# Kernel optimization log

Hardware: AMD Instinct MI355X
Metric: run time of the kernel (lower is better)

Reference implementation:

```python
import jax, jax.numpy as jnp
import numpy as np

N = 50000      # nodes
E = 1000000    # directed edges
G = 1000       # graphs (molecules) in the batch
D_NODE = 133
D_EDGE = 147
D_H = 128
D_OUT = 1


def _lrelu(v):
    # torch.nn.functional.leaky_relu default negative_slope = 0.01
    return jnp.where(v >= 0, v, 0.01 * v)


def setup_inputs() -> dict:
    key = jax.random.key(0)
    ks = jax.random.split(key, 10)
    s = 0.05
    return {
        "x": jax.random.normal(ks[0], (N, D_NODE), jnp.float32),
        "concat_feats": jax.random.normal(ks[1], (E, D_EDGE), jnp.float32),
        "srt_concat_batch": jax.random.randint(ks[2], (E,), 0, N),
        "end_concat_batch": jax.random.randint(ks[3], (E,), 0, N),
        "num_concat_feats": E,
        "batch": jnp.sort(jax.random.randint(ks[4], (N,), 0, G)),
        "W_init": s * jax.random.normal(ks[5], (D_H, D_EDGE), jnp.float32),
        "b_init": jnp.zeros((D_H,), jnp.float32),
        "W_h1": s * jax.random.normal(ks[6], (D_H, D_H), jnp.float32),
        "b_h1": jnp.zeros((D_H,), jnp.float32),
        "W_mol": s * jax.random.normal(ks[7], (D_H, D_H), jnp.float32),
        "b_mol": jnp.zeros((D_H,), jnp.float32),
        "W_out": s * jax.random.normal(ks[8], (D_OUT, D_H), jnp.float32),
        "b_out": jnp.zeros((D_OUT,), jnp.float32),
    }


def reference(x, concat_feats, srt_concat_batch, end_concat_batch,
              num_concat_feats, batch,
              W_init, b_init, W_h1, b_h1, W_mol, b_mol, W_out, b_out):
    n = x.shape[0]

    def mp(h):
        # scatter_add over end nodes, gather at srt nodes, subtract reverse contribution
        agg = jax.ops.segment_sum(h, end_concat_batch, num_segments=n)
        return agg[srt_concat_batch] - h[end_concat_batch]

    h0 = _lrelu(concat_feats @ W_init.T + b_init)                 # [E, D_H]
    h1 = _lrelu(h0 + mp(h0) @ W_h1.T + b_h1)
    h2 = _lrelu(h1 + mp(h1) @ W_h1.T + b_h1)
    h3 = _lrelu(h2 + mp(h2) @ W_h1.T + b_h1)

    h_node = jax.ops.segment_sum(h3, srt_concat_batch, num_segments=n)  # [N, D_H]
    atom_embs = _lrelu(h_node @ W_mol.T + b_mol)
    # F.normalize(p=2, dim=1) with eps=1e-12
    norms = jnp.maximum(jnp.linalg.norm(atom_embs, axis=1, keepdims=True), 1e-12)
    hg = jax.ops.segment_sum(atom_embs / norms, batch, num_segments=G)  # [G, D_H]
    out = hg @ W_out.T + b_out                                          # [G, D_OUT]
    return (out, atom_embs)
```

## Files before the change

### kernel.cpp

```cpp
#include <hip/hip_runtime.h>

#define NN 50000
#define NE 1000000
#define NG 1000
#define KE 147
#define DH 128

using u16 = unsigned short;
typedef __attribute__((ext_vector_type(8))) short bf16x8;
typedef __attribute__((ext_vector_type(4))) float f32x4;

__device__ __forceinline__ float lrelu(float v){ return fmaxf(v, 0.01f*v); }
__device__ __forceinline__ float bf2f(u16 u){ unsigned int x = ((unsigned int)u)<<16; float f; __builtin_memcpy(&f,&x,4); return f; }
__device__ __forceinline__ u16 f2bf(float f){ unsigned int x; __builtin_memcpy(&x,&f,4); x += 0x7fffu + ((x>>16)&1u); return (u16)(x>>16); }
__device__ __forceinline__ float bflo(unsigned w){ unsigned x = w<<16; float f; __builtin_memcpy(&f,&x,4); return f; }
__device__ __forceinline__ float bfhi(unsigned w){ unsigned x = w & 0xffff0000u; float f; __builtin_memcpy(&f,&x,4); return f; }
__device__ __forceinline__ unsigned pk2(float lo, float hi){ return ((unsigned)f2bf(hi)<<16) | (unsigned)f2bf(lo); }
__device__ __host__ __forceinline__ int cpi(int p){ return (p & 64) | ((p & 3) << 4) | ((p & 63) >> 2); }

__global__ __launch_bounds__(256) void hist_kernel(const int* __restrict__ endi, const int* __restrict__ srt,
                                                   int* __restrict__ cntE, int* __restrict__ cntS){
  for (int i = blockIdx.x*256 + threadIdx.x; i < NE; i += gridDim.x*256){
    atomicAdd(&cntE[endi[i]], 1);
    atomicAdd(&cntS[srt[i]], 1);
  }
}

__global__ __launch_bounds__(1024) void scan2_kernel(const int* __restrict__ cntE, int* __restrict__ offE,
                                                     const int* __restrict__ cntS, int* __restrict__ offS){
  const int* deg = blockIdx.x ? cntS : cntE;
  int* off = blockIdx.x ? offS : offE;
  __shared__ int wsum[17];
  const int t = threadIdx.x, lane = t & 63, wv = t >> 6;
  int carry = 0;
  for (int base = 0; base < 50176; base += 1024){
    const int i = base + t;
    int v = (i < NN) ? deg[i] : 0;
    int s = v;
    #pragma unroll
    for (int d = 1; d < 64; d <<= 1){
      int x = __shfl_up(s, d);
      if (lane >= d) s += x;
    }
    if (lane == 63) wsum[wv] = s;
    __syncthreads();
    if (t == 0){
      int run = 0;
      #pragma unroll
      for (int k = 0; k < 16; ++k){ int x = wsum[k]; wsum[k] = run; run += x; }
      wsum[16] = run;
    }
    __syncthreads();
    if (i <= NN) off[i] = carry + wsum[wv] + s - v;
    carry += wsum[16];
    __syncthreads();
  }
}

__global__ __launch_bounds__(256) void scatter_kernel(const int* __restrict__ endi, const int* __restrict__ srt,
                                                      int* __restrict__ curE, int* __restrict__ curS,
                                                      int* __restrict__ rankE, int* __restrict__ srtE,
                                                      int* __restrict__ listS2, int* __restrict__ endS){
  for (int i = blockIdx.x*256 + threadIdx.x; i < NE; i += gridDim.x*256){
    const int e = endi[i], s = srt[i];
    int p = atomicAdd(&curE[e], 1);
    rankE[i] = p; srtE[p] = s;
    int q = atomicAdd(&curS[s], 1);
    listS2[q] = p; endS[q] = e;
  }
}

__global__ __launch_bounds__(256) void convertW_kernel(const float* __restrict__ W1, const float* __restrict__ W0,
                                                       const float* __restrict__ b0, const float* __restrict__ b1,
                                                       u16* __restrict__ Wb1, u16* __restrict__ Wb0,
                                                       float* __restrict__ bp0, float* __restrict__ bp1){
  int i = blockIdx.x*256 + threadIdx.x;
  if (i < 128*128){
    int j = i >> 7, k = i & 127;
    Wb1[i] = f2bf(W1[j*DH + cpi(k)]);
  }
  if (i < 128*160){
    int j = i/160, k = i - j*160;
    Wb0[i] = (k < KE) ? f2bf(W0[j*KE + k]) : (u16)0;
  }
  if (i < 128){ bp0[i] = b0[cpi(i)]; bp1[i] = b1[cpi(i)]; }
}

__global__ __launch_bounds__(256) void layer0_mfma(const float* __restrict__ cf, const u16* __restrict__ Wb0,
                                                   const float* __restrict__ bp0, const int* __restrict__ rankE,
                                                   u16* __restrict__ h){
  __shared__ __align__(16) u16 As[64*168];
  const int t = threadIdx.x, lane = t & 63, wv = t >> 6;
  const int wr = wv >> 1, wc = wv & 1;
  const int e0 = blockIdx.x * 64;
  const int q = lane & 15, kg8 = (lane >> 4)*8;

  bf16x8 bfrag[5][4];
  #pragma unroll
  for (int fc = 0; fc < 4; ++fc)
    #pragma unroll
    for (int ks = 0; ks < 5; ++ks)
      bfrag[ks][fc] = *(const bf16x8*)&Wb0[(size_t)(wc*64 + fc*16 + q)*160 + ks*32 + kg8];

  {
    const float4* src = (const float4*)(cf + (size_t)e0*KE);
    #pragma unroll
    for (int k = 0; k < 10; ++k){
      const int i4 = t + k*256;
      if (i4 < 2352){
        float4 v = src[i4];
        const int g = i4*4;
        int r = (unsigned)g / 147u;
        int c = g - r*147;
        u16 w0 = f2bf(v.x), w1 = f2bf(v.y), w2 = f2bf(v.z), w3 = f2bf(v.w);
        As[r*168 + c] = w0; if (++c == 147){ c = 0; ++r; }
        As[r*168 + c] = w1; if (++c == 147){ c = 0; ++r; }
        As[r*168 + c] = w2; if (++c == 147){ c = 0; ++r; }
        As[r*168 + c] = w3;
      }
    }
  }
  for (int idx = t; idx < 64*16; idx += 256){
    const int r = idx >> 4, c = idx & 15;
    if (c < 13) As[r*168 + 147 + c] = 0;
  }
  __syncthreads();

  f32x4 acc[2][4];
  #pragma unroll
  for (int fr = 0; fr < 2; ++fr)
    #pragma unroll
    for (int fc = 0; fc < 4; ++fc){ acc[fr][fc][0]=0.f; acc[fr][fc][1]=0.f; acc[fr][fc][2]=0.f; acc[fr][fc][3]=0.f; }
  #pragma unroll
  for (int ks = 0; ks < 5; ++ks){
    bf16x8 a[2];
    #pragma unroll
    for (int fr = 0; fr < 2; ++fr)
      a[fr] = *(const bf16x8*)&As[(wr*32 + fr*16 + q)*168 + ks*32 + kg8];
    #pragma unroll
    for (int fr = 0; fr < 2; ++fr)
      #pragma unroll
      for (int fc = 0; fc < 4; ++fc)
        acc[fr][fc] = __builtin_amdgcn_mfma_f32_16x16x32_bf16(a[fr], bfrag[ks][fc], acc[fr][fc], 0, 0, 0);
  }

  const float4 bb = *(const float4*)&bp0[wc*64 + q*4];
  #pragma unroll
  for (int fr = 0; fr < 2; ++fr){
    #pragma unroll
    for (int r = 0; r < 4; ++r){
      const int ee = e0 + wr*32 + fr*16 + (lane>>4)*4 + r;
      const int row = rankE[ee];
      ushort4 o;
      o.x = f2bf(lrelu(acc[fr][0][r] + bb.x));
      o.y = f2bf(lrelu(acc[fr][1][r] + bb.y));
      o.z = f2bf(lrelu(acc[fr][2][r] + bb.z));
      o.w = f2bf(lrelu(acc[fr][3][r] + bb.w));
      *(ushort4*)&h[(size_t)row*DH + wc*64 + q*4] = o;
    }
  }
}

__global__ __launch_bounds__(256) void aggE_kernel(const u16* __restrict__ h, const int* __restrict__ off,
                                                   float* __restrict__ agg){
  const int t = threadIdx.x, lane = t & 63, wv = t >> 6;
  const int n = blockIdx.x*2 + (wv >> 1);
  const int half = wv & 1;
  const int lo = off[n], hi = off[n+1];
  const int c8 = half*64 + (lane & 7)*8, sub = lane >> 3;
  float a0=0,a1=0,a2=0,a3=0,a4=0,a5=0,a6=0,a7=0;
  for (int i = lo + sub; i < hi; i += 8){
    uint4 hv = *(const uint4*)&h[(size_t)i*DH + c8];
    a0 += bflo(hv.x); a1 += bfhi(hv.x); a2 += bflo(hv.y); a3 += bfhi(hv.y);
    a4 += bflo(hv.z); a5 += bfhi(hv.z); a6 += bflo(hv.w); a7 += bfhi(hv.w);
  }
  a0 += __shfl_xor(a0,8);  a1 += __shfl_xor(a1,8);  a2 += __shfl_xor(a2,8);  a3 += __shfl_xor(a3,8);
  a4 += __shfl_xor(a4,8);  a5 += __shfl_xor(a5,8);  a6 += __shfl_xor(a6,8);  a7 += __shfl_xor(a7,8);
  a0 += __shfl_xor(a0,16); a1 += __shfl_xor(a1,16); a2 += __shfl_xor(a2,16); a3 += __shfl_xor(a3,16);
  a4 += __shfl_xor(a4,16); a5 += __shfl_xor(a5,16); a6 += __shfl_xor(a6,16); a7 += __shfl_xor(a7,16);
  a0 += __shfl_xor(a0,32); a1 += __shfl_xor(a1,32); a2 += __shfl_xor(a2,32); a3 += __shfl_xor(a3,32);
  a4 += __shfl_xor(a4,32); a5 += __shfl_xor(a5,32); a6 += __shfl_xor(a6,32); a7 += __shfl_xor(a7,32);
  if (sub == 0){
    *(float4*)&agg[(size_t)n*DH + c8]     = make_float4(a0,a1,a2,a3);
    *(float4*)&agg[(size_t)n*DH + c8 + 4] = make_float4(a4,a5,a6,a7);
  }
}

__global__ __launch_bounds__(256) void pq_gemm(const float* __restrict__ agg, const u16* __restrict__ h,
                                               const int* __restrict__ rankE, const u16* __restrict__ Wb1,
                                               const float* __restrict__ bp1, u16* __restrict__ P,
                                               u16* __restrict__ Q){
  __shared__ u16 Alds[128][136];
  const int t = threadIdx.x, lane = t & 63, wv = t >> 6;
  const int wr = wv >> 1, wc = wv & 1;
  const int r0 = blockIdx.x * 128;
  const int q = lane & 15, kg8 = (lane >> 4)*8;

  bf16x8 bfrag[4][4];
  #pragma unroll
  for (int fc = 0; fc < 4; ++fc)
    #pragma unroll
    for (int ks = 0; ks < 4; ++ks)
      bfrag[ks][fc] = *(const bf16x8*)&Wb1[(size_t)(wc*64 + fc*16 + q)*128 + ks*32 + kg8];

  {
    const int rt = t >> 1, half = t & 1;
    const int gr = r0 + rt;
    u16* dst = &Alds[rt][half*64];
    if (gr < NN){
      const float4* src = (const float4*)&agg[(size_t)gr*DH + half*64];
      #pragma unroll
      for (int p = 0; p < 16; ++p){
        float4 x = src[p];
        ushort4 o; o.x=f2bf(x.x); o.y=f2bf(x.y); o.z=f2bf(x.z); o.w=f2bf(x.w);
        *(ushort4*)&dst[p*4] = o;
      }
    } else if (gr < 2*NN){
      const int row = rankE[gr - NN];
      const ushort4* src = (const ushort4*)&h[(size_t)row*DH + half*64];
      #pragma unroll
      for (int p = 0; p < 16; ++p) *(ushort4*)&dst[p*4] = src[p];
    } else {
      ushort4 z; z.x=0; z.y=0; z.z=0; z.w=0;
      #pragma unroll
      for (int p = 0; p < 16; ++p) *(ushort4*)&dst[p*4] = z;
    }
  }
  __syncthreads();

  f32x4 acc[4][4];
  #pragma unroll
  for (int fr = 0; fr < 4; ++fr)
    #pragma unroll
    for (int fc = 0; fc < 4; ++fc){ acc[fr][fc][0]=0.f; acc[fr][fc][1]=0.f; acc[fr][fc][2]=0.f; acc[fr][fc][3]=0.f; }
  #pragma unroll
  for (int ks = 0; ks < 4; ++ks){
    bf16x8 a[4];
    #pragma unroll
    for (int fr = 0; fr < 4; ++fr)
      a[fr] = *(const bf16x8*)&Alds[wr*64 + fr*16 + q][ks*32 + kg8];
    #pragma unroll
    for (int fr = 0; fr < 4; ++fr)
      #pragma unroll
      for (int fc = 0; fc < 4; ++fc)
        acc[fr][fc] = __builtin_amdgcn_mfma_f32_16x16x32_bf16(a[fr], bfrag[ks][fc], acc[fr][fc], 0, 0, 0);
  }

  const float4 bb = *(const float4*)&bp1[wc*64 + q*4];
  #pragma unroll
  for (int fr = 0; fr < 4; ++fr){
    #pragma unroll
    for (int r = 0; r < 4; ++r){
      const int grow = r0 + wr*64 + fr*16 + (lane>>4)*4 + r;
      if (grow < NN){
        ushort4 o;
        o.x = f2bf(acc[fr][0][r] + bb.x);
        o.y = f2bf(acc[fr][1][r] + bb.y);
        o.z = f2bf(acc[fr][2][r] + bb.z);
        o.w = f2bf(acc[fr][3][r] + bb.w);
        *(ushort4*)&P[(size_t)grow*DH + wc*64 + q*4] = o;
      } else if (grow < 2*NN){
        ushort4 o;
        o.x = f2bf(acc[fr][0][r]);
        o.y = f2bf(acc[fr][1][r]);
        o.z = f2bf(acc[fr][2][r]);
        o.w = f2bf(acc[fr][3][r]);
        *(ushort4*)&Q[(size_t)(grow-NN)*DH + wc*64 + q*4] = o;
      }
    }
  }
}

__global__ __launch_bounds__(256) void fused_mid(u16* __restrict__ h, const u16* __restrict__ P,
                                                 const u16* __restrict__ Q, const int* __restrict__ srtE,
                                                 const int* __restrict__ off, float* __restrict__ agg){
  const int t = threadIdx.x, lane = t & 63, wv = t >> 6;
  const int n = blockIdx.x*2 + (wv >> 1);
  const int half = wv & 1;
  const int lo = off[n], hi = off[n+1];
  const int c8 = half*64 + (lane & 7)*8, sub = lane >> 3;
  const uint4 qw = *(const uint4*)&Q[(size_t)n*DH + c8];
  const float q0 = bflo(qw.x), q1 = bfhi(qw.x), q2 = bflo(qw.y), q3 = bfhi(qw.y);
  const float q4 = bflo(qw.z), q5 = bfhi(qw.z), q6 = bflo(qw.w), q7 = bfhi(qw.w);
  float a0=0,a1=0,a2=0,a3=0,a4=0,a5=0,a6=0,a7=0;
  for (int i = lo + sub; i < hi; i += 8){
    const int s = srtE[i];
    uint4 hv = *(const uint4*)&h[(size_t)i*DH + c8];
    uint4 pw = *(const uint4*)&P[(size_t)s*DH + c8];
    float v0 = lrelu(bflo(hv.x) + bflo(pw.x) - q0);
    float v1 = lrelu(bfhi(hv.x) + bfhi(pw.x) - q1);
    float v2 = lrelu(bflo(hv.y) + bflo(pw.y) - q2);
    float v3 = lrelu(bfhi(hv.y) + bfhi(pw.y) - q3);
    float v4 = lrelu(bflo(hv.z) + bflo(pw.z) - q4);
    float v5 = lrelu(bfhi(hv.z) + bfhi(pw.z) - q5);
    float v6 = lrelu(bflo(hv.w) + bflo(pw.w) - q6);
    float v7 = lrelu(bfhi(hv.w) + bfhi(pw.w) - q7);
    uint4 o;
    o.x = pk2(v0, v1); o.y = pk2(v2, v3); o.z = pk2(v4, v5); o.w = pk2(v6, v7);
    *(uint4*)&h[(size_t)i*DH + c8] = o;
    a0+=v0; a1+=v1; a2+=v2; a3+=v3; a4+=v4; a5+=v5; a6+=v6; a7+=v7;
  }
  a0 += __shfl_xor(a0,8);  a1 += __shfl_xor(a1,8);  a2 += __shfl_xor(a2,8);  a3 += __shfl_xor(a3,8);
  a4 += __shfl_xor(a4,8);  a5 += __shfl_xor(a5,8);  a6 += __shfl_xor(a6,8);  a7 += __shfl_xor(a7,8);
  a0 += __shfl_xor(a0,16); a1 += __shfl_xor(a1,16); a2 += __shfl_xor(a2,16); a3 += __shfl_xor(a3,16);
  a4 += __shfl_xor(a4,16); a5 += __shfl_xor(a5,16); a6 += __shfl_xor(a6,16); a7 += __shfl_xor(a7,16);
  a0 += __shfl_xor(a0,32); a1 += __shfl_xor(a1,32); a2 += __shfl_xor(a2,32); a3 += __shfl_xor(a3,32);
  a4 += __shfl_xor(a4,32); a5 += __shfl_xor(a5,32); a6 += __shfl_xor(a6,32); a7 += __shfl_xor(a7,32);
  if (sub == 0){
    *(float4*)&agg[(size_t)n*DH + c8]     = make_float4(a0,a1,a2,a3);
    *(float4*)&agg[(size_t)n*DH + c8 + 4] = make_float4(a4,a5,a6,a7);
  }
}

__global__ __launch_bounds__(256) void fused_last(const u16* __restrict__ h, const u16* __restrict__ P,
                                                  const u16* __restrict__ Q, const int* __restrict__ endS,
                                                  const int* __restrict__ listS2, const int* __restrict__ off,
                                                  float* __restrict__ hnode){
  const int t = threadIdx.x, lane = t & 63, wv = t >> 6;
  const int s = blockIdx.x*2 + (wv >> 1);
  const int half = wv & 1;
  const int lo = off[s], hi = off[s+1];
  const int c8 = half*64 + (lane & 7)*8, sub = lane >> 3;
  const uint4 pw = *(const uint4*)&P[(size_t)s*DH + c8];
  const float p0 = bflo(pw.x), p1 = bfhi(pw.x), p2 = bflo(pw.y), p3 = bfhi(pw.y);
  const float p4 = bflo(pw.z), p5 = bfhi(pw.z), p6 = bflo(pw.w), p7 = bfhi(pw.w);
  float a0=0,a1=0,a2=0,a3=0,a4=0,a5=0,a6=0,a7=0;
  for (int i = lo + sub; i < hi; i += 8){
    const int row = listS2[i];
    const int d = endS[i];
    uint4 hv = *(const uint4*)&h[(size_t)row*DH + c8];
    uint4 qw = *(const uint4*)&Q[(size_t)d*DH + c8];
    a0 += lrelu(bflo(hv.x) + p0 - bflo(qw.x));
    a1 += lrelu(bfhi(hv.x) + p1 - bfhi(qw.x));
    a2 += lrelu(bflo(hv.y) + p2 - bflo(qw.y));
    a3 += lrelu(bfhi(hv.y) + p3 - bfhi(qw.y));
    a4 += lrelu(bflo(hv.z) + p4 - bflo(qw.z));
    a5 += lrelu(bfhi(hv.z) + p5 - bfhi(qw.z));
    a6 += lrelu(bflo(hv.w) + p6 - bflo(qw.w));
    a7 += lrelu(bfhi(hv.w) + p7 - bfhi(qw.w));
  }
  a0 += __shfl_xor(a0,8);  a1 += __shfl_xor(a1,8);  a2 += __shfl_xor(a2,8);  a3 += __shfl_xor(a3,8);
  a4 += __shfl_xor(a4,8);  a5 += __shfl_xor(a5,8);  a6 += __shfl_xor(a6,8);  a7 += __shfl_xor(a7,8);
  a0 += __shfl_xor(a0,16); a1 += __shfl_xor(a1,16); a2 += __shfl_xor(a2,16); a3 += __shfl_xor(a3,16);
  a4 += __shfl_xor(a4,16); a5 += __shfl_xor(a5,16); a6 += __shfl_xor(a6,16); a7 += __shfl_xor(a7,16);
  a0 += __shfl_xor(a0,32); a1 += __shfl_xor(a1,32); a2 += __shfl_xor(a2,32); a3 += __shfl_xor(a3,32);
  a4 += __shfl_xor(a4,32); a5 += __shfl_xor(a5,32); a6 += __shfl_xor(a6,32); a7 += __shfl_xor(a7,32);
  if (sub == 0){
    *(float4*)&hnode[(size_t)s*DH + c8]     = make_float4(a0,a1,a2,a3);
    *(float4*)&hnode[(size_t)s*DH + c8 + 4] = make_float4(a4,a5,a6,a7);
  }
}

__global__ __launch_bounds__(256) void node_kernel(
    const float* __restrict__ hn, const float* __restrict__ W,
    const float* __restrict__ b, float* __restrict__ atom, float* __restrict__ normed)
{
  __shared__ float Wt[64*132];
  __shared__ float ms[32*DH];
  const int t = threadIdx.x;
  const int r0 = blockIdx.x * 32;
  const int jg = t & 31, eg = t >> 5;
  for (int idx = t; idx < 32*DH; idx += 256) {
    const int r = r0 + (idx >> 7);
    ms[idx] = (r < NN) ? hn[(size_t)r*DH + (idx & 127)] : 0.f;
  }
  float acc[4][4] = {};
  for (int c = 0; c < 2; ++c) {
    __syncthreads();
    for (int idx = t; idx < 128*64; idx += 256) {
      const int j = idx >> 6, kl = idx & 63;
      Wt[kl*132 + j] = W[j*DH + c*64 + ((kl&3)*16 + (kl>>2))];
    }
    __syncthreads();
    #pragma unroll 4
    for (int kl = 0; kl < 64; ++kl) {
      const float4 w = *(const float4*)&Wt[kl*132 + jg*4];
      const int kg = c*64 + kl;
      #pragma unroll
      for (int i = 0; i < 4; ++i) {
        const float mv = ms[(eg*4+i)*DH + kg];
        acc[i][0] += mv*w.x; acc[i][1] += mv*w.y; acc[i][2] += mv*w.z; acc[i][3] += mv*w.w;
      }
    }
  }
  float bj[4];
  #pragma unroll
  for (int c2 = 0; c2 < 4; ++c2) bj[c2] = b[jg*4 + c2];
  #pragma unroll
  for (int i = 0; i < 4; ++i) {
    const int r = r0 + eg*4 + i;
    float v[4]; float ss = 0.f;
    #pragma unroll
    for (int c2 = 0; c2 < 4; ++c2) { v[c2] = lrelu(acc[i][c2] + bj[c2]); ss += v[c2]*v[c2]; }
    ss += __shfl_xor(ss, 1); ss += __shfl_xor(ss, 2); ss += __shfl_xor(ss, 4);
    ss += __shfl_xor(ss, 8); ss += __shfl_xor(ss, 16);
    if (r < NN) {
      *(float4*)&atom[(size_t)r*DH + jg*4] = make_float4(v[0],v[1],v[2],v[3]);
      const float inv = 1.f / fmaxf(sqrtf(ss), 1e-12f);
      *(float4*)&normed[(size_t)r*DH + jg*4] = make_float4(v[0]*inv,v[1]*inv,v[2]*inv,v[3]*inv);
    }
  }
}

__global__ __launch_bounds__(128) void graph_out_kernel(const float* __restrict__ normed, const int* __restrict__ batch,
                                                        const float* __restrict__ Wo, const float* __restrict__ bo,
                                                        float* __restrict__ out){
  const int g = blockIdx.x, t = threadIdx.x;
  int lo, hi;
  { int a=0, bb=NN; while(a<bb){ int m=(a+bb)>>1; if (batch[m] < g) a=m+1; else bb=m; } lo=a; }
  { int a=lo, bb=NN; while(a<bb){ int m=(a+bb)>>1; if (batch[m] < g+1) a=m+1; else bb=m; } hi=a; }
  float s = 0.f;
  for (int n = lo; n < hi; ++n) s += normed[(size_t)n*DH + t];
  float v = s * Wo[t];
  #pragma unroll
  for (int d2 = 1; d2 < 64; d2 <<= 1) v += __shfl_xor(v, d2);
  __shared__ float red[2];
  if ((t & 63) == 0) red[t >> 6] = v;
  __syncthreads();
  if (t == 0) out[g] = red[0] + red[1] + bo[0];
}

extern "C" void kernel_launch(void* const* d_in, const int* in_sizes, int n_in,
                              void* d_out, int out_size, void* d_ws, size_t ws_size,
                              hipStream_t stream)
{
  const float* cf     = (const float*)d_in[1];
  const int*   srt    = (const int*)d_in[2];
  const int*   endi   = (const int*)d_in[3];
  const int*   batch  = (const int*)d_in[5];
  const float* W_init = (const float*)d_in[6];
  const float* b_init = (const float*)d_in[7];
  const float* W_h1   = (const float*)d_in[8];
  const float* b_h1   = (const float*)d_in[9];
  const float* W_mol  = (const float*)d_in[10];
  const float* b_mol  = (const float*)d_in[11];
  const float* W_out  = (const float*)d_in[12];
  const float* b_out  = (const float*)d_in[13];

  float* out  = (float*)d_out;
  float* atom = out + NG;

  char* ws = (char*)d_ws;
  u16*   h      = (u16*)(ws);
  float* agg    = (float*)(ws + 256000000);
  u16*   P      = (u16*)(ws + 281600000);
  u16*   Q      = (u16*)(ws + 307200000);
  int*   srtE   = (int*)(ws + 332800000);
  int*   endS   = (int*)(ws + 336800000);
  int*   rankE  = (int*)(ws + 340800000);
  int*   listS2 = (int*)(ws + 344800000);
  int*   offE   = (int*)(ws + 348800000);
  int*   offS   = (int*)(ws + 349000704);
  int*   curE   = (int*)(ws + 349201408);
  int*   curS   = (int*)(ws + 349402112);
  u16*   Wb1    = (u16*)(ws + 349602816);
  u16*   Wb0    = (u16*)(ws + 349635584);
  float* bp0    = (float*)(ws + 349676544);
  float* bp1    = (float*)(ws + 349677056);
  float* hnode  = agg;
  float* normed = (float*)(ws);

  hipMemsetAsync(curE, 0, 200704, stream);
  hipMemsetAsync(curS, 0, 200704, stream);
  hist_kernel<<<1024, 256, 0, stream>>>(endi, srt, curE, curS);
  scan2_kernel<<<2, 1024, 0, stream>>>(curE, offE, curS, offS);
  hipMemcpyAsync(curE, offE, (size_t)NN*4, hipMemcpyDeviceToDevice, stream);
  hipMemcpyAsync(curS, offS, (size_t)NN*4, hipMemcpyDeviceToDevice, stream);
  scatter_kernel<<<1024, 256, 0, stream>>>(endi, srt, curE, curS, rankE, srtE, listS2, endS);
  convertW_kernel<<<80, 256, 0, stream>>>(W_h1, W_init, b_init, b_h1, Wb1, Wb0, bp0, bp1);

  layer0_mfma<<<NE/64, 256, 0, stream>>>(cf, Wb0, bp0, rankE, h);
  aggE_kernel<<<NN/2, 256, 0, stream>>>(h, offE, agg);

  for (int l = 0; l < 2; ++l){
    pq_gemm<<<(2*NN + 127)/128, 256, 0, stream>>>(agg, h, rankE, Wb1, bp1, P, Q);
    fused_mid<<<NN/2, 256, 0, stream>>>(h, P, Q, srtE, offE, agg);
  }
  pq_gemm<<<(2*NN + 127)/128, 256, 0, stream>>>(agg, h, rankE, Wb1, bp1, P, Q);
  fused_last<<<NN/2, 256, 0, stream>>>(h, P, Q, endS, listS2, offS, hnode);

  node_kernel<<<(NN + 31)/32, 256, 0, stream>>>(hnode, W_mol, b_mol, atom, normed);
  graph_out_kernel<<<NG, 128, 0, stream>>>(normed, batch, W_out, b_out, out);
}
```

Baseline: 1.038 ms.

## Skip h2 writeback, recompute it on the fly; MFMA node GEMM with atomic graph pooling

```diff
diff --git a/kernel.cpp b/kernel.cpp
--- a/kernel.cpp
+++ b/kernel.cpp
@@ -71,13 +71,16 @@
 }
 
 __global__ __launch_bounds__(256) void convertW_kernel(const float* __restrict__ W1, const float* __restrict__ W0,
+                                                       const float* __restrict__ Wm,
                                                        const float* __restrict__ b0, const float* __restrict__ b1,
                                                        u16* __restrict__ Wb1, u16* __restrict__ Wb0,
+                                                       u16* __restrict__ Wbm,
                                                        float* __restrict__ bp0, float* __restrict__ bp1){
   int i = blockIdx.x*256 + threadIdx.x;
   if (i < 128*128){
     int j = i >> 7, k = i & 127;
     Wb1[i] = f2bf(W1[j*DH + cpi(k)]);
+    Wbm[i] = f2bf(Wm[j*DH + cpi(k)]);
   }
   if (i < 128*160){
     int j = i/160, k = i - j*160;
@@ -220,6 +223,104 @@
       const ushort4* src = (const ushort4*)&h[(size_t)row*DH + half*64];
       #pragma unroll
       for (int p = 0; p < 16; ++p) *(ushort4*)&dst[p*4] = src[p];
+    } else {
+      ushort4 z; z.x=0; z.y=0; z.z=0; z.w=0;
+      #pragma unroll
+      for (int p = 0; p < 16; ++p) *(ushort4*)&dst[p*4] = z;
+    }
+  }
+  __syncthreads();
+
+  f32x4 acc[4][4];
+  #pragma unroll
+  for (int fr = 0; fr < 4; ++fr)
+    #pragma unroll
+    for (int fc = 0; fc < 4; ++fc){ acc[fr][fc][0]=0.f; acc[fr][fc][1]=0.f; acc[fr][fc][2]=0.f; acc[fr][fc][3]=0.f; }
+  #pragma unroll
+  for (int ks = 0; ks < 4; ++ks){
+    bf16x8 a[4];
+    #pragma unroll
+    for (int fr = 0; fr < 4; ++fr)
+      a[fr] = *(const bf16x8*)&Alds[wr*64 + fr*16 + q][ks*32 + kg8];
+    #pragma unroll
+    for (int fr = 0; fr < 4; ++fr)
+      #pragma unroll
+      for (int fc = 0; fc < 4; ++fc)
+        acc[fr][fc] = __builtin_amdgcn_mfma_f32_16x16x32_bf16(a[fr], bfrag[ks][fc], acc[fr][fc], 0, 0, 0);
+  }
+
+  const float4 bb = *(const float4*)&bp1[wc*64 + q*4];
+  #pragma unroll
+  for (int fr = 0; fr < 4; ++fr){
+    #pragma unroll
+    for (int r = 0; r < 4; ++r){
+      const int grow = r0 + wr*64 + fr*16 + (lane>>4)*4 + r;
+      if (grow < NN){
+        ushort4 o;
+        o.x = f2bf(acc[fr][0][r] + bb.x);
+        o.y = f2bf(acc[fr][1][r] + bb.y);
+        o.z = f2bf(acc[fr][2][r] + bb.z);
+        o.w = f2bf(acc[fr][3][r] + bb.w);
+        *(ushort4*)&P[(size_t)grow*DH + wc*64 + q*4] = o;
+      } else if (grow < 2*NN){
+        ushort4 o;
+        o.x = f2bf(acc[fr][0][r]);
+        o.y = f2bf(acc[fr][1][r]);
+        o.z = f2bf(acc[fr][2][r]);
+        o.w = f2bf(acc[fr][3][r]);
+        *(ushort4*)&Q[(size_t)(grow-NN)*DH + wc*64 + q*4] = o;
+      }
+    }
+  }
+}
+
+__global__ __launch_bounds__(256) void pq_gemm3(const float* __restrict__ agg, const u16* __restrict__ h1,
+                                                const int* __restrict__ rankE, const int* __restrict__ srt,
+                                                const int* __restrict__ endi,
+                                                const u16* __restrict__ P2, const u16* __restrict__ Q2,
+                                                const u16* __restrict__ Wb1, const float* __restrict__ bp1,
+                                                u16* __restrict__ P, u16* __restrict__ Q){
+  __shared__ u16 Alds[128][136];
+  const int t = threadIdx.x, lane = t & 63, wv = t >> 6;
+  const int wr = wv >> 1, wc = wv & 1;
+  const int r0 = blockIdx.x * 128;
+  const int q = lane & 15, kg8 = (lane >> 4)*8;
+
+  bf16x8 bfrag[4][4];
+  #pragma unroll
+  for (int fc = 0; fc < 4; ++fc)
+    #pragma unroll
+    for (int ks = 0; ks < 4; ++ks)
+      bfrag[ks][fc] = *(const bf16x8*)&Wb1[(size_t)(wc*64 + fc*16 + q)*128 + ks*32 + kg8];
+
+  {
+    const int rt = t >> 1, half = t & 1;
+    const int gr = r0 + rt;
+    u16* dst = &Alds[rt][half*64];
+    if (gr < NN){
+      const float4* src = (const float4*)&agg[(size_t)gr*DH + half*64];
+      #pragma unroll
+      for (int p = 0; p < 16; ++p){
+        float4 x = src[p];
+        ushort4 o; o.x=f2bf(x.x); o.y=f2bf(x.y); o.z=f2bf(x.z); o.w=f2bf(x.w);
+        *(ushort4*)&dst[p*4] = o;
+      }
+    } else if (gr < 2*NN){
+      const int e = gr - NN;
+      const int row = rankE[e], s = srt[e], d = endi[e];
+      const ushort4* hsrc = (const ushort4*)&h1[(size_t)row*DH + half*64];
+      const ushort4* psrc = (const ushort4*)&P2[(size_t)s*DH + half*64];
+      const ushort4* qsrc = (const ushort4*)&Q2[(size_t)d*DH + half*64];
+      #pragma unroll
+      for (int p = 0; p < 16; ++p){
+        ushort4 hv = hsrc[p], pv = psrc[p], qv = qsrc[p];
+        ushort4 o;
+        o.x = f2bf(lrelu(bf2f(hv.x) + bf2f(pv.x) - bf2f(qv.x)));
+        o.y = f2bf(lrelu(bf2f(hv.y) + bf2f(pv.y) - bf2f(qv.y)));
+        o.z = f2bf(lrelu(bf2f(hv.z) + bf2f(pv.z) - bf2f(qv.z)));
+        o.w = f2bf(lrelu(bf2f(hv.w) + bf2f(pv.w) - bf2f(qv.w)));
+        *(ushort4*)&dst[p*4] = o;
+      }
     } else {
       ushort4 z; z.x=0; z.y=0; z.z=0; z.w=0;
       #pragma unroll
@@ -312,32 +413,82 @@
   }
 }
 
-__global__ __launch_bounds__(256) void fused_last(const u16* __restrict__ h, const u16* __restrict__ P,
-                                                  const u16* __restrict__ Q, const int* __restrict__ endS,
-                                                  const int* __restrict__ listS2, const int* __restrict__ off,
-                                                  float* __restrict__ hnode){
+__global__ __launch_bounds__(256) void fused_mid_nw(const u16* __restrict__ h, const u16* __restrict__ P,
+                                                    const u16* __restrict__ Q, const int* __restrict__ srtE,
+                                                    const int* __restrict__ off, float* __restrict__ agg){
+  const int t = threadIdx.x, lane = t & 63, wv = t >> 6;
+  const int n = blockIdx.x*2 + (wv >> 1);
+  const int half = wv & 1;
+  const int lo = off[n], hi = off[n+1];
+  const int c8 = half*64 + (lane & 7)*8, sub = lane >> 3;
+  const uint4 qw = *(const uint4*)&Q[(size_t)n*DH + c8];
+  const float q0 = bflo(qw.x), q1 = bfhi(qw.x), q2 = bflo(qw.y), q3 = bfhi(qw.y);
+  const float q4 = bflo(qw.z), q5 = bfhi(qw.z), q6 = bflo(qw.w), q7 = bfhi(qw.w);
+  float a0=0,a1=0,a2=0,a3=0,a4=0,a5=0,a6=0,a7=0;
+  for (int i = lo + sub; i < hi; i += 8){
+    const int s = srtE[i];
+    uint4 hv = *(const uint4*)&h[(size_t)i*DH + c8];
+    uint4 pw = *(const uint4*)&P[(size_t)s*DH + c8];
+    a0 += lrelu(bflo(hv.x) + bflo(pw.x) - q0);
+    a1 += lrelu(bfhi(hv.x) + bfhi(pw.x) - q1);
+    a2 += lrelu(bflo(hv.y) + bflo(pw.y) - q2);
+    a3 += lrelu(bfhi(hv.y) + bfhi(pw.y) - q3);
+    a4 += lrelu(bflo(hv.z) + bflo(pw.z) - q4);
+    a5 += lrelu(bfhi(hv.z) + bfhi(pw.z) - q5);
+    a6 += lrelu(bflo(hv.w) + bflo(pw.w) - q6);
+    a7 += lrelu(bfhi(hv.w) + bfhi(pw.w) - q7);
+  }
+  a0 += __shfl_xor(a0,8);  a1 += __shfl_xor(a1,8);  a2 += __shfl_xor(a2,8);  a3 += __shfl_xor(a3,8);
+  a4 += __shfl_xor(a4,8);  a5 += __shfl_xor(a5,8);  a6 += __shfl_xor(a6,8);  a7 += __shfl_xor(a7,8);
+  a0 += __shfl_xor(a0,16); a1 += __shfl_xor(a1,16); a2 += __shfl_xor(a2,16); a3 += __shfl_xor(a3,16);
+  a4 += __shfl_xor(a4,16); a5 += __shfl_xor(a5,16); a6 += __shfl_xor(a6,16); a7 += __shfl_xor(a7,16);
+  a0 += __shfl_xor(a0,32); a1 += __shfl_xor(a1,32); a2 += __shfl_xor(a2,32); a3 += __shfl_xor(a3,32);
+  a4 += __shfl_xor(a4,32); a5 += __shfl_xor(a5,32); a6 += __shfl_xor(a6,32); a7 += __shfl_xor(a7,32);
+  if (sub == 0){
+    *(float4*)&agg[(size_t)n*DH + c8]     = make_float4(a0,a1,a2,a3);
+    *(float4*)&agg[(size_t)n*DH + c8 + 4] = make_float4(a4,a5,a6,a7);
+  }
+}
+
+__global__ __launch_bounds__(256) void fused_last3(const u16* __restrict__ h1,
+                                                   const u16* __restrict__ P2, const u16* __restrict__ Q2,
+                                                   const u16* __restrict__ P3, const u16* __restrict__ Q3,
+                                                   const int* __restrict__ endS, const int* __restrict__ listS2,
+                                                   const int* __restrict__ off, float* __restrict__ hnode){
   const int t = threadIdx.x, lane = t & 63, wv = t >> 6;
   const int s = blockIdx.x*2 + (wv >> 1);
   const int half = wv & 1;
   const int lo = off[s], hi = off[s+1];
   const int c8 = half*64 + (lane & 7)*8, sub = lane >> 3;
-  const uint4 pw = *(const uint4*)&P[(size_t)s*DH + c8];
-  const float p0 = bflo(pw.x), p1 = bfhi(pw.x), p2 = bflo(pw.y), p3 = bfhi(pw.y);
-  const float p4 = bflo(pw.z), p5 = bfhi(pw.z), p6 = bflo(pw.w), p7 = bfhi(pw.w);
+  const uint4 p2w = *(const uint4*)&P2[(size_t)s*DH + c8];
+  const uint4 p3w = *(const uint4*)&P3[(size_t)s*DH + c8];
+  const float p20 = bflo(p2w.x), p21 = bfhi(p2w.x), p22 = bflo(p2w.y), p23 = bfhi(p2w.y);
+  const float p24 = bflo(p2w.z), p25 = bfhi(p2w.z), p26 = bflo(p2w.w), p27 = bfhi(p2w.w);
+  const float p30 = bflo(p3w.x), p31 = bfhi(p3w.x), p32 = bflo(p3w.y), p33 = bfhi(p3w.y);
+  const float p34 = bflo(p3w.z), p35 = bfhi(p3w.z), p36 = bflo(p3w.w), p37 = bfhi(p3w.w);
   float a0=0,a1=0,a2=0,a3=0,a4=0,a5=0,a6=0,a7=0;
   for (int i = lo + sub; i < hi; i += 8){
     const int row = listS2[i];
     const int d = endS[i];
-    uint4 hv = *(const uint4*)&h[(size_t)row*DH + c8];
-    uint4 qw = *(const uint4*)&Q[(size_t)d*DH + c8];
-    a0 += lrelu(bflo(hv.x) + p0 - bflo(qw.x));
-    a1 += lrelu(bfhi(hv.x) + p1 - bfhi(qw.x));
-    a2 += lrelu(bflo(hv.y) + p2 - bflo(qw.y));
-    a3 += lrelu(bfhi(hv.y) + p3 - bfhi(qw.y));
-    a4 += lrelu(bflo(hv.z) + p4 - bflo(qw.z));
-    a5 += lrelu(bfhi(hv.z) + p5 - bfhi(qw.z));
-    a6 += lrelu(bflo(hv.w) + p6 - bflo(qw.w));
-    a7 += lrelu(bfhi(hv.w) + p7 - bfhi(qw.w));
+    uint4 hv = *(const uint4*)&h1[(size_t)row*DH + c8];
+    uint4 q2w = *(const uint4*)&Q2[(size_t)d*DH + c8];
+    uint4 q3w = *(const uint4*)&Q3[(size_t)d*DH + c8];
+    float t0 = lrelu(bflo(hv.x) + p20 - bflo(q2w.x));
+    float t1 = lrelu(bfhi(hv.x) + p21 - bfhi(q2w.x));
+    float t2 = lrelu(bflo(hv.y) + p22 - bflo(q2w.y));
+    float t3 = lrelu(bfhi(hv.y) + p23 - bfhi(q2w.y));
+    float t4 = lrelu(bflo(hv.z) + p24 - bflo(q2w.z));
+    float t5 = lrelu(bfhi(hv.z) + p25 - bfhi(q2w.z));
+    float t6 = lrelu(bflo(hv.w) + p26 - bflo(q2w.w));
+    float t7 = lrelu(bfhi(hv.w) + p27 - bfhi(q2w.w));
+    a0 += lrelu(t0 + p30 - bflo(q3w.x));
+    a1 += lrelu(t1 + p31 - bfhi(q3w.x));
+    a2 += lrelu(t2 + p32 - bflo(q3w.y));
+    a3 += lrelu(t3 + p33 - bfhi(q3w.y));
+    a4 += lrelu(t4 + p34 - bflo(q3w.z));
+    a5 += lrelu(t5 + p35 - bfhi(q3w.z));
+    a6 += lrelu(t6 + p36 - bflo(q3w.w));
+    a7 += lrelu(t7 + p37 - bfhi(q3w.w));
   }
   a0 += __shfl_xor(a0,8);  a1 += __shfl_xor(a1,8);  a2 += __shfl_xor(a2,8);  a3 += __shfl_xor(a3,8);
   a4 += __shfl_xor(a4,8);  a5 += __shfl_xor(a5,8);  a6 += __shfl_xor(a6,8);  a7 += __shfl_xor(a7,8);
@@ -351,67 +502,121 @@
   }
 }
 
-__global__ __launch_bounds__(256) void node_kernel(
-    const float* __restrict__ hn, const float* __restrict__ W,
-    const float* __restrict__ b, float* __restrict__ atom, float* __restrict__ normed)
-{
-  __shared__ float Wt[64*132];
-  __shared__ float ms[32*DH];
-  const int t = threadIdx.x;
-  const int r0 = blockIdx.x * 32;
-  const int jg = t & 31, eg = t >> 5;
-  for (int idx = t; idx < 32*DH; idx += 256) {
-    const int r = r0 + (idx >> 7);
-    ms[idx] = (r < NN) ? hn[(size_t)r*DH + (idx & 127)] : 0.f;
-  }
-  float acc[4][4] = {};
-  for (int c = 0; c < 2; ++c) {
-    __syncthreads();
-    for (int idx = t; idx < 128*64; idx += 256) {
-      const int j = idx >> 6, kl = idx & 63;
-      Wt[kl*132 + j] = W[j*DH + c*64 + ((kl&3)*16 + (kl>>2))];
-    }
-    __syncthreads();
-    #pragma unroll 4
-    for (int kl = 0; kl < 64; ++kl) {
-      const float4 w = *(const float4*)&Wt[kl*132 + jg*4];
-      const int kg = c*64 + kl;
-      #pragma unroll
-      for (int i = 0; i < 4; ++i) {
-        const float mv = ms[(eg*4+i)*DH + kg];
-        acc[i][0] += mv*w.x; acc[i][1] += mv*w.y; acc[i][2] += mv*w.z; acc[i][3] += mv*w.w;
-      }
-    }
-  }
-  float bj[4];
-  #pragma unroll
-  for (int c2 = 0; c2 < 4; ++c2) bj[c2] = b[jg*4 + c2];
-  #pragma unroll
-  for (int i = 0; i < 4; ++i) {
-    const int r = r0 + eg*4 + i;
-    float v[4]; float ss = 0.f;
-    #pragma unroll
-    for (int c2 = 0; c2 < 4; ++c2) { v[c2] = lrelu(acc[i][c2] + bj[c2]); ss += v[c2]*v[c2]; }
-    ss += __shfl_xor(ss, 1); ss += __shfl_xor(ss, 2); ss += __shfl_xor(ss, 4);
-    ss += __shfl_xor(ss, 8); ss += __shfl_xor(ss, 16);
-    if (r < NN) {
-      *(float4*)&atom[(size_t)r*DH + jg*4] = make_float4(v[0],v[1],v[2],v[3]);
-      const float inv = 1.f / fmaxf(sqrtf(ss), 1e-12f);
-      *(float4*)&normed[(size_t)r*DH + jg*4] = make_float4(v[0]*inv,v[1]*inv,v[2]*inv,v[3]*inv);
-    }
-  }
-}
-
-__global__ __launch_bounds__(128) void graph_out_kernel(const float* __restrict__ normed, const int* __restrict__ batch,
-                                                        const float* __restrict__ Wo, const float* __restrict__ bo,
-                                                        float* __restrict__ out){
+__global__ __launch_bounds__(256) void node_mfma(const float* __restrict__ hn, const u16* __restrict__ Wbm,
+                                                 const float* __restrict__ bm, const int* __restrict__ batch,
+                                                 float* __restrict__ atom, float* __restrict__ hg){
+  __shared__ u16 Alds[128][136];
+  __shared__ float ssb[128];
+  const int t = threadIdx.x, lane = t & 63, wv = t >> 6;
+  const int wr = wv >> 1, wc = wv & 1;
+  const int r0 = blockIdx.x * 128;
+  const int q = lane & 15, kg8 = (lane >> 4)*8;
+
+  bf16x8 bfrag[4][4];
+  #pragma unroll
+  for (int fc = 0; fc < 4; ++fc)
+    #pragma unroll
+    for (int ks = 0; ks < 4; ++ks)
+      bfrag[ks][fc] = *(const bf16x8*)&Wbm[(size_t)(wc*64 + fc*16 + q)*128 + ks*32 + kg8];
+
+  {
+    const int rt = t >> 1, half = t & 1;
+    const int gr = r0 + rt;
+    u16* dst = &Alds[rt][half*64];
+    if (gr < NN){
+      const float4* src = (const float4*)&hn[(size_t)gr*DH + half*64];
+      #pragma unroll
+      for (int p = 0; p < 16; ++p){
+        float4 x = src[p];
+        ushort4 o; o.x=f2bf(x.x); o.y=f2bf(x.y); o.z=f2bf(x.z); o.w=f2bf(x.w);
+        *(ushort4*)&dst[p*4] = o;
+      }
+    } else {
+      ushort4 z; z.x=0; z.y=0; z.z=0; z.w=0;
+      #pragma unroll
+      for (int p = 0; p < 16; ++p) *(ushort4*)&dst[p*4] = z;
+    }
+  }
+  if (t < 128) ssb[t] = 0.f;
+  __syncthreads();
+
+  f32x4 acc[4][4];
+  #pragma unroll
+  for (int fr = 0; fr < 4; ++fr)
+    #pragma unroll
+    for (int fc = 0; fc < 4; ++fc){ acc[fr][fc][0]=0.f; acc[fr][fc][1]=0.f; acc[fr][fc][2]=0.f; acc[fr][fc][3]=0.f; }
+  #pragma unroll
+  for (int ks = 0; ks < 4; ++ks){
+    bf16x8 a[4];
+    #pragma unroll
+    for (int fr = 0; fr < 4; ++fr)
+      a[fr] = *(const bf16x8*)&Alds[wr*64 + fr*16 + q][ks*32 + kg8];
+    #pragma unroll
+    for (int fr = 0; fr < 4; ++fr)
+      #pragma unroll
+      for (int fc = 0; fc < 4; ++fc)
+        acc[fr][fc] = __builtin_amdgcn_mfma_f32_16x16x32_bf16(a[fr], bfrag[ks][fc], acc[fr][fc], 0, 0, 0);
+  }
+
+  float bmv[4];
+  #pragma unroll
+  for (int fc = 0; fc < 4; ++fc) bmv[fc] = bm[wc*64 + fc*16 + q];
+
+  float sp[4][4];
+  #pragma unroll
+  for (int fr = 0; fr < 4; ++fr)
+    #pragma unroll
+    for (int r = 0; r < 4; ++r){
+      float s2 = 0.f;
+      #pragma unroll
+      for (int fc = 0; fc < 4; ++fc){
+        float v = lrelu(acc[fr][fc][r] + bmv[fc]);
+        acc[fr][fc][r] = v;
+        s2 += v*v;
+      }
+      sp[fr][r] = s2;
+    }
+  #pragma unroll
+  for (int m = 1; m <= 8; m <<= 1)
+    #pragma unroll
+    for (int fr = 0; fr < 4; ++fr)
+      #pragma unroll
+      for (int r = 0; r < 4; ++r)
+        sp[fr][r] += __shfl_xor(sp[fr][r], m);
+  if ((lane & 15) == 0){
+    #pragma unroll
+    for (int fr = 0; fr < 4; ++fr)
+      #pragma unroll
+      for (int r = 0; r < 4; ++r)
+        atomicAdd(&ssb[wr*64 + fr*16 + (lane>>4)*4 + r], sp[fr][r]);
+  }
+  __syncthreads();
+
+  #pragma unroll
+  for (int fr = 0; fr < 4; ++fr){
+    #pragma unroll
+    for (int r = 0; r < 4; ++r){
+      const int lrow = wr*64 + fr*16 + (lane>>4)*4 + r;
+      const int grow = r0 + lrow;
+      if (grow < NN){
+        const float inv = 1.f / fmaxf(sqrtf(ssb[lrow]), 1e-12f);
+        const int g = batch[grow];
+        #pragma unroll
+        for (int fc = 0; fc < 4; ++fc){
+          const int col = wc*64 + fc*16 + q;
+          const float v = acc[fr][fc][r];
+          atom[(size_t)grow*DH + col] = v;
+          atomicAdd(&hg[(size_t)g*DH + col], v*inv);
+        }
+      }
+    }
+  }
+}
+
+__global__ __launch_bounds__(128) void out_gemv(const float* __restrict__ hg, const float* __restrict__ Wo,
+                                                const float* __restrict__ bo, float* __restrict__ out){
   const int g = blockIdx.x, t = threadIdx.x;
-  int lo, hi;
-  { int a=0, bb=NN; while(a<bb){ int m=(a+bb)>>1; if (batch[m] < g) a=m+1; else bb=m; } lo=a; }
-  { int a=lo, bb=NN; while(a<bb){ int m=(a+bb)>>1; if (batch[m] < g+1) a=m+1; else bb=m; } hi=a; }
-  float s = 0.f;
-  for (int n = lo; n < hi; ++n) s += normed[(size_t)n*DH + t];
-  float v = s * Wo[t];
+  float v = hg[(size_t)g*DH + t] * Wo[t];
   #pragma unroll
   for (int d2 = 1; d2 < 64; d2 <<= 1) v += __shfl_xor(v, d2);
   __shared__ float red[2];
@@ -443,8 +648,10 @@
   char* ws = (char*)d_ws;
   u16*   h      = (u16*)(ws);
   float* agg    = (float*)(ws + 256000000);
-  u16*   P      = (u16*)(ws + 281600000);
-  u16*   Q      = (u16*)(ws + 307200000);
+  u16*   Pa     = (u16*)(ws + 281600000);
+  u16*   Qa     = (u16*)(ws + 294400000);
+  u16*   Pb     = (u16*)(ws + 307200000);
+  u16*   Qb     = (u16*)(ws + 320000000);
   int*   srtE   = (int*)(ws + 332800000);
   int*   endS   = (int*)(ws + 336800000);
   int*   rankE  = (int*)(ws + 340800000);
@@ -455,30 +662,34 @@
   int*   curS   = (int*)(ws + 349402112);
   u16*   Wb1    = (u16*)(ws + 349602816);
   u16*   Wb0    = (u16*)(ws + 349635584);
-  float* bp0    = (float*)(ws + 349676544);
-  float* bp1    = (float*)(ws + 349677056);
+  u16*   Wbm    = (u16*)(ws + 349676544);
+  float* bp0    = (float*)(ws + 349709312);
+  float* bp1    = (float*)(ws + 349709824);
+  float* hg     = (float*)(ws + 349710336);
   float* hnode  = agg;
-  float* normed = (float*)(ws);
 
   hipMemsetAsync(curE, 0, 200704, stream);
   hipMemsetAsync(curS, 0, 200704, stream);
+  hipMemsetAsync(hg, 0, (size_t)NG*DH*4, stream);
   hist_kernel<<<1024, 256, 0, stream>>>(endi, srt, curE, curS);
   scan2_kernel<<<2, 1024, 0, stream>>>(curE, offE, curS, offS);
   hipMemcpyAsync(curE, offE, (size_t)NN*4, hipMemcpyDeviceToDevice, stream);
   hipMemcpyAsync(curS, offS, (size_t)NN*4, hipMemcpyDeviceToDevice, stream);
   scatter_kernel<<<1024, 256, 0, stream>>>(endi, srt, curE, curS, rankE, srtE, listS2, endS);
-  convertW_kernel<<<80, 256, 0, stream>>>(W_h1, W_init, b_init, b_h1, Wb1, Wb0, bp0, bp1);
+  convertW_kernel<<<80, 256, 0, stream>>>(W_h1, W_init, W_mol, b_init, b_h1, Wb1, Wb0, Wbm, bp0, bp1);
 
   layer0_mfma<<<NE/64, 256, 0, stream>>>(cf, Wb0, bp0, rankE, h);
   aggE_kernel<<<NN/2, 256, 0, stream>>>(h, offE, agg);
 
-  for (int l = 0; l < 2; ++l){
-    pq_gemm<<<(2*NN + 127)/128, 256, 0, stream>>>(agg, h, rankE, Wb1, bp1, P, Q);
-    fused_mid<<<NN/2, 256, 0, stream>>>(h, P, Q, srtE, offE, agg);
-  }
-  pq_gemm<<<(2*NN + 127)/128, 256, 0, stream>>>(agg, h, rankE, Wb1, bp1, P, Q);
-  fused_last<<<NN/2, 256, 0, stream>>>(h, P, Q, endS, listS2, offS, hnode);
-
-  node_kernel<<<(NN + 31)/32, 256, 0, stream>>>(hnode, W_mol, b_mol, atom, normed);
-  graph_out_kernel<<<NG, 128, 0, stream>>>(normed, batch, W_out, b_out, out);
-}
+  pq_gemm<<<(2*NN + 127)/128, 256, 0, stream>>>(agg, h, rankE, Wb1, bp1, Pa, Qa);
+  fused_mid<<<NN/2, 256, 0, stream>>>(h, Pa, Qa, srtE, offE, agg);
+
+  pq_gemm<<<(2*NN + 127)/128, 256, 0, stream>>>(agg, h, rankE, Wb1, bp1, Pb, Qb);
+  fused_mid_nw<<<NN/2, 256, 0, stream>>>(h, Pb, Qb, srtE, offE, agg);
+
+  pq_gemm3<<<(2*NN + 127)/128, 256, 0, stream>>>(agg, h, rankE, srt, endi, Pb, Qb, Wb1, bp1, Pa, Qa);
+  fused_last3<<<NN/2, 256, 0, stream>>>(h, Pb, Qb, Pa, Qa, endS, listS2, offS, hnode);
+
+  node_mfma<<<(NN + 127)/128, 256, 0, stream>>>(hnode, Wbm, b_mol, batch, atom, hg);
+  out_gemv<<<NG, 128, 0, stream>>>(hg, W_out, b_out, out);
+}
```

After: 1.037 ms, median of 2. Within noise of the previous version (-0.1%).
